# Kernel optimization log

Measured on AMD Instinct MI355X. Metric: run time of the kernel, lower is better.

Reference implementation:

```python
import jax, jax.numpy as jnp
import numpy as np

# Hierarchy: 3 levels with 50 / 500 / 5000 classes, branching factor 10.
PIQUETS = (0, 50, 550, 5550)  # cumulative offsets per level
NB_LEVELS = 3
BATCH = 4096


def _make_parent():
    """parent[j] = global index of the parent of global node j (0 for roots).
    Encodes the same structure as the dense H matrix (H[p, j] = 1 iff parent[j] == p)."""
    parent = np.zeros(PIQUETS[-1], dtype=np.int32)
    parent[PIQUETS[1]:PIQUETS[2]] = np.arange(500) // 10            # level-1 -> level-0
    parent[PIQUETS[2]:PIQUETS[3]] = PIQUETS[1] + np.arange(5000) // 10  # level-2 -> level-1
    return jnp.asarray(parent)


def setup_inputs() -> dict:
    key = jax.random.key(0)
    k1, k2 = jax.random.split(key)
    y_pred = jax.random.normal(k1, (BATCH, PIQUETS[-1]), dtype=jnp.float32)
    target = jax.random.randint(k2, (BATCH,), 0, 5000)  # local leaf-level indices
    return {"y_pred": y_pred, "target": target, "parent": _make_parent()}


def reference(y_pred, target, parent):
    # children_preds[b, p] = sum of child logits of node p
    # == (H[:piquets[-2], :] @ y_pred.T).T, exploiting H's one-parent sparsity.
    children = jax.ops.segment_sum(
        y_pred.T[PIQUETS[1]:], parent[PIQUETS[1]:], num_segments=PIQUETS[-2]
    ).T  # (B, piquets[-2])

    levels_pred = [y_pred[:, PIQUETS[k]:PIQUETS[k + 1]] for k in range(NB_LEVELS)]
    levels_children = [children[:, PIQUETS[k]:PIQUETS[k + 1]] for k in range(NB_LEVELS - 1)]
    log_p = [jax.nn.log_softmax(l, axis=1) for l in levels_pred]
    log_c = [jax.nn.log_softmax(l, axis=1) for l in levels_children]

    # Ancestor targets per level (vectorized replacement for get_grandparents loops)
    g = target.astype(jnp.int32) + PIQUETS[-2]  # global leaf index
    globs = [g]
    for _ in range(NB_LEVELS - 1):
        globs.append(parent[globs[-1]])
    globs = globs[::-1]  # level 0 .. level L-1, global indices
    loc = [globs[k] - PIQUETS[k] for k in range(NB_LEVELS)]  # local per-level targets

    def ce(logp, tgt):
        return -jnp.take_along_axis(logp, tgt[:, None], axis=1).mean()

    def kl_mean(logp, logq):
        # torch KLDivLoss(reduction='mean'): mean over ALL elements of q*(log q - log p)
        return jnp.mean(jnp.exp(logq) * (logq - logp))

    loss = jnp.float32(0.0)
    kl_penalty = jnp.float32(0.0)
    for k in range(NB_LEVELS - 1):
        kl_penalty += 0.5 * (kl_mean(log_p[k], log_c[k]) + kl_mean(log_c[k], log_p[k]))
        loss += 0.5 * ce(log_p[k], loc[k])
    loss += 0.5 * ce(log_p[-1], loc[-1])
    loss += 0.5 * kl_penalty
    return loss
```

## Files before the change

kernel.cpp:

```cpp
#include <hip/hip_runtime.h>

#define BATCH 4096
#define ROW   5550

__device__ __forceinline__ float wave_sum(float v) {
    #pragma unroll
    for (int off = 32; off; off >>= 1) v += __shfl_xor(v, off, 64);
    return v;
}

__global__ __launch_bounds__(256)
void hjsd_kernel(const float* __restrict__ y, const int* __restrict__ tgt,
                 float* __restrict__ rowout) {
    __shared__ __align__(16) float s0[56];
    __shared__ __align__(16) float s1[504];
    __shared__ __align__(16) float s2[5504];
    __shared__ float scr[36];

    const int b   = blockIdx.x;
    const int tid = threadIdx.x;

    const float2* prow = reinterpret_cast<const float2*>(y + (size_t)b * ROW);
    for (int i = tid; i < ROW / 2; i += 256) {
        float2 v = prow[i];
        int e = 2 * i;
        if (e >= 550) {
            int f   = e - 550;
            int idx = f + 2 * (f / 20);
            s2[idx] = v.x; s2[idx + 1] = v.y;
        } else if (e >= 50) {
            s1[e - 50] = v.x; s1[e - 49] = v.y;
        } else {
            s0[e] = v.x; s0[e + 1] = v.y;
        }
    }
    __syncthreads();

    float E2 = 0.f, EC1 = 0.f, E1 = 0.f, EC0 = 0.f, E0 = 0.f;
    float S11 = 0.f, S21 = 0.f, S10 = 0.f, S20 = 0.f;

    if (tid < 250) {
        const float2* p2 = reinterpret_cast<const float2*>(s2 + 22 * tid);
        float v[20];
        #pragma unroll
        for (int j = 0; j < 10; ++j) { float2 t2 = p2[j]; v[2*j] = t2.x; v[2*j+1] = t2.y; }
        float c0 = 0.f, c1 = 0.f;
        #pragma unroll
        for (int j = 0; j < 10; ++j) c0 += v[j];
        #pragma unroll
        for (int j = 0; j < 10; ++j) c1 += v[10 + j];
        #pragma unroll
        for (int j = 0; j < 20; ++j) E2 += __expf(v[j]);
        float ec0 = __expf(c0), ec1 = __expf(c1);
        EC1 = ec0 + ec1;
        float xa = s1[2 * tid], xb = s1[2 * tid + 1];
        float ea = __expf(xa), eb = __expf(xb);
        E1  = ea + eb;
        S11 = ec0 * (c0 - xa) + ec1 * (c1 - xb);
        S21 = ea * (xa - c0) + eb * (xb - c1);
    }

    if (tid < 50) {
        const float2* p1 = reinterpret_cast<const float2*>(s1 + 10 * tid);
        float c = 0.f;
        #pragma unroll
        for (int j = 0; j < 5; ++j) { float2 t2 = p1[j]; c += t2.x + t2.y; }
        float ec = __expf(c);
        float x0 = s0[tid];
        float e0 = __expf(x0);
        EC0 = ec; E0 = e0;
        S10 = ec * (c - x0);
        S20 = e0 * (x0 - c);
    }

    float sums[9] = {E2, EC1, E1, EC0, E0, S11, S21, S10, S20};
    #pragma unroll
    for (int k = 0; k < 9; ++k) sums[k] = wave_sum(sums[k]);
    const int wid = tid >> 6;
    if ((tid & 63) == 0) {
        #pragma unroll
        for (int k = 0; k < 9; ++k) scr[wid * 9 + k] = sums[k];
    }
    __syncthreads();

    if (tid == 0) {
        float t9[9];
        #pragma unroll
        for (int k = 0; k < 9; ++k)
            t9[k] = scr[k] + scr[9 + k] + scr[18 + k] + scr[27 + k];
        float L2 = __logf(t9[0]), L1 = __logf(t9[2]), L0 = __logf(t9[4]);
        int t = tgt[b];
        float y2 = s2[t + 2 * (t / 20)];
        float y1 = s1[t / 10];
        float y0 = s0[t / 100];
        float ce = (L2 - y2) + (L1 - y1) + (L0 - y0);
        float kl = (0.25f / 500.0f) * (t9[5] / t9[1] + t9[6] / t9[2])
                 + (0.25f / 50.0f)  * (t9[7] / t9[3] + t9[8] / t9[4]);
        rowout[b] = 0.5f * ce + kl;
    }
}

__global__ __launch_bounds__(256)
void reduce_kernel(const float* __restrict__ rows, float* __restrict__ out) {
    __shared__ float scr[4];
    const int tid = threadIdx.x;
    const float4* p = reinterpret_cast<const float4*>(rows);
    float s = 0.0f;
    for (int i = tid; i < BATCH / 4; i += 256) {
        float4 v = p[i];
        s += v.x + v.y + v.z + v.w;
    }
    s = wave_sum(s);
    if ((tid & 63) == 0) scr[tid >> 6] = s;
    __syncthreads();
    if (tid == 0) out[0] = (scr[0] + scr[1] + scr[2] + scr[3]) * (1.0f / BATCH);
}

extern "C" void kernel_launch(void* const* d_in, const int* in_sizes, int n_in,
                              void* d_out, int out_size, void* d_ws, size_t ws_size,
                              hipStream_t stream) {
    const float* y   = (const float*)d_in[0];
    const int*   tgt = (const int*)d_in[1];
    float* out    = (float*)d_out;
    float* rowbuf = (float*)d_ws;

    hjsd_kernel<<<BATCH, 256, 0, stream>>>(y, tgt, rowbuf);
    reduce_kernel<<<1, 256, 0, stream>>>(rowbuf, out);
}
```

Before: 146.9 us.

## Stage rows into LDS with direct global-to-LDS 16-byte loads

```diff
diff --git a/kernel.cpp b/kernel.cpp
--- a/kernel.cpp
+++ b/kernel.cpp
@@ -2,6 +2,9 @@
 
 #define BATCH 4096
 #define ROW   5550
+
+typedef const __attribute__((address_space(1))) void glb_void;
+typedef __attribute__((address_space(3))) void lds_void;
 
 __device__ __forceinline__ float wave_sum(float v) {
     #pragma unroll
@@ -12,35 +15,38 @@
 __global__ __launch_bounds__(256)
 void hjsd_kernel(const float* __restrict__ y, const int* __restrict__ tgt,
                  float* __restrict__ rowout) {
-    __shared__ __align__(16) float s0[56];
-    __shared__ __align__(16) float s1[504];
-    __shared__ __align__(16) float s2[5504];
+    __shared__ __align__(16) float s_buf[5552];
     __shared__ float scr[36];
 
-    const int b   = blockIdx.x;
-    const int tid = threadIdx.x;
+    const int b    = blockIdx.x;
+    const int tid  = threadIdx.x;
+    const int w    = tid >> 6;
+    const int lane = tid & 63;
 
-    const float2* prow = reinterpret_cast<const float2*>(y + (size_t)b * ROW);
-    for (int i = tid; i < ROW / 2; i += 256) {
-        float2 v = prow[i];
-        int e = 2 * i;
-        if (e >= 550) {
-            int f   = e - 550;
-            int idx = f + 2 * (f / 20);
-            s2[idx] = v.x; s2[idx + 1] = v.y;
-        } else if (e >= 50) {
-            s1[e - 50] = v.x; s1[e - 49] = v.y;
-        } else {
-            s0[e] = v.x; s0[e + 1] = v.y;
+    const float* yrow  = y + (size_t)b * ROW;
+    const int    ofs   = (b & 1) ? 2 : 0;
+    const float* gbase = yrow - ofs;
+
+    for (int c = w; c < 22; c += 4) {
+        int d = 256 * c + 4 * lane;
+        if (d < 5552) {
+            __builtin_amdgcn_global_load_lds((glb_void*)(gbase + d),
+                                             (lds_void*)(s_buf + 256 * c),
+                                             16, 0, 0);
         }
     }
+    asm volatile("s_waitcnt vmcnt(0)" ::: "memory");
     __syncthreads();
+
+    const float* s_row = s_buf + ofs;
+    const float* s1    = s_row + 50;
+    const float* s2    = s_row + 550;
 
     float E2 = 0.f, EC1 = 0.f, E1 = 0.f, EC0 = 0.f, E0 = 0.f;
     float S11 = 0.f, S21 = 0.f, S10 = 0.f, S20 = 0.f;
 
     if (tid < 250) {
-        const float2* p2 = reinterpret_cast<const float2*>(s2 + 22 * tid);
+        const float2* p2 = reinterpret_cast<const float2*>(s2 + 20 * tid);
         float v[20];
         #pragma unroll
         for (int j = 0; j < 10; ++j) { float2 t2 = p2[j]; v[2*j] = t2.x; v[2*j+1] = t2.y; }
@@ -53,11 +59,11 @@
         for (int j = 0; j < 20; ++j) E2 += __expf(v[j]);
         float ec0 = __expf(c0), ec1 = __expf(c1);
         EC1 = ec0 + ec1;
-        float xa = s1[2 * tid], xb = s1[2 * tid + 1];
-        float ea = __expf(xa), eb = __expf(xb);
+        float2 xab = *reinterpret_cast<const float2*>(s1 + 2 * tid);
+        float ea = __expf(xab.x), eb = __expf(xab.y);
         E1  = ea + eb;
-        S11 = ec0 * (c0 - xa) + ec1 * (c1 - xb);
-        S21 = ea * (xa - c0) + eb * (xb - c1);
+        S11 = ec0 * (c0 - xab.x) + ec1 * (c1 - xab.y);
+        S21 = ea * (xab.x - c0) + eb * (xab.y - c1);
     }
 
     if (tid < 50) {
@@ -66,7 +72,7 @@
         #pragma unroll
         for (int j = 0; j < 5; ++j) { float2 t2 = p1[j]; c += t2.x + t2.y; }
         float ec = __expf(c);
-        float x0 = s0[tid];
+        float x0 = s_row[tid];
         float e0 = __expf(x0);
         EC0 = ec; E0 = e0;
         S10 = ec * (c - x0);
@@ -76,10 +82,9 @@
     float sums[9] = {E2, EC1, E1, EC0, E0, S11, S21, S10, S20};
     #pragma unroll
     for (int k = 0; k < 9; ++k) sums[k] = wave_sum(sums[k]);
-    const int wid = tid >> 6;
-    if ((tid & 63) == 0) {
+    if (lane == 0) {
         #pragma unroll
-        for (int k = 0; k < 9; ++k) scr[wid * 9 + k] = sums[k];
+        for (int k = 0; k < 9; ++k) scr[w * 9 + k] = sums[k];
     }
     __syncthreads();
 
@@ -90,10 +95,7 @@
             t9[k] = scr[k] + scr[9 + k] + scr[18 + k] + scr[27 + k];
         float L2 = __logf(t9[0]), L1 = __logf(t9[2]), L0 = __logf(t9[4]);
         int t = tgt[b];
-        float y2 = s2[t + 2 * (t / 20)];
-        float y1 = s1[t / 10];
-        float y0 = s0[t / 100];
-        float ce = (L2 - y2) + (L1 - y1) + (L0 - y0);
+        float ce = (L2 - s2[t]) + (L1 - s1[t / 10]) + (L0 - s_row[t / 100]);
         float kl = (0.25f / 500.0f) * (t9[5] / t9[1] + t9[6] / t9[2])
                  + (0.25f / 50.0f)  * (t9[7] / t9[3] + t9[8] / t9[4]);
         rowout[b] = 0.5f * ce + kl;
@@ -106,8 +108,9 @@
     const int tid = threadIdx.x;
     const float4* p = reinterpret_cast<const float4*>(rows);
     float s = 0.0f;
-    for (int i = tid; i < BATCH / 4; i += 256) {
-        float4 v = p[i];
+    #pragma unroll
+    for (int i = 0; i < 4; ++i) {
+        float4 v = p[tid + 256 * i];
         s += v.x + v.y + v.z + v.w;
     }
     s = wave_sum(s);
```

Result: faster. 137.2 us (-6.7%).
